# Kernel tuning notes

Hardware: AMD Instinct MI355X
Metric: run time of the kernel (lower is better)

## Reference

```python
import jax, jax.numpy as jnp
import numpy as np

IMG = 416
NC = 80
B = 32
NOBJ = 20          # objects placed per image
K = 32             # fixed max GT boxes per image for ignore-mask IoU (>= NOBJ)
THR = 0.5
ANCHORS = np.array([[10,13],[16,30],[33,23],[30,61],[62,45],[59,119],
                    [116,90],[156,198],[373,326]], np.float32)


def _bce(logits, targets):
    # elementwise binary_cross_entropy_with_logits
    return jnp.maximum(logits, 0.0) - logits * targets + jnp.log1p(jnp.exp(-jnp.abs(logits)))


def _make_y_true(key, batch, G, nc, img, nobj):
    N = G * G * 3
    k1, k2, k3, k4 = jax.random.split(key, 4)
    idx = jax.random.randint(k1, (batch, nobj), 0, N)
    xy = jax.random.uniform(k2, (batch, nobj, 2), jnp.float32) * img
    wh = jax.random.uniform(k3, (batch, nobj, 2), jnp.float32) * 90.0 + 10.0
    cls = jax.random.randint(k4, (batch, nobj), 0, nc)
    y = jnp.zeros((batch, N, 5 + nc), jnp.float32)
    b = jnp.arange(batch)[:, None]
    y = y.at[b, idx, 0].set(xy[..., 0])
    y = y.at[b, idx, 1].set(xy[..., 1])
    y = y.at[b, idx, 2].set(wh[..., 0])
    y = y.at[b, idx, 3].set(wh[..., 1])
    y = y.at[b, idx, 4].set(1.0)
    y = y.at[b, idx, 5 + cls].set(1.0)
    return y.reshape(batch, G, G, 3, 5 + nc)


def setup_inputs() -> dict:
    key = jax.random.key(0)
    ks = jax.random.split(key, 6)
    inp = {}
    for i, G in enumerate([13, 26, 52]):
        inp[f"fm{i}"] = jax.random.normal(ks[i], (B, 3 * (5 + NC), G, G), jnp.float32)
        inp[f"yt{i}"] = _make_y_true(ks[3 + i], B, G, NC, IMG, NOBJ)
    inp["anchors"] = jnp.asarray(ANCHORS)
    return inp


def _predict_transform(fm, anchors3):
    batch, ch, G, _ = fm.shape
    A = 3
    stride = IMG // G
    bbox = 5 + NC
    # [B, A*bbox, G*G] -> [B, G*G, A*bbox] -> [B, G, G, A, bbox]
    p = fm.reshape(batch, A * bbox, G * G).transpose(0, 2, 1).reshape(batch, G, G, A, bbox)
    box_centers = jax.nn.sigmoid(p[..., 0:2])
    box_sizes_raw = p[..., 2:4]
    conf_logits = p[..., 4:5]
    prob_logits = p[..., 5:]
    ar = jnp.arange(G, dtype=fm.dtype)
    gy, gx = jnp.meshgrid(ar, ar, indexing='ij')       # row, col
    xy_offset = jnp.stack([gx, gy], axis=-1).reshape(G, G, 1, 2)
    box_centers = (box_centers + xy_offset) * stride
    box_sizes = jnp.exp(box_sizes_raw) * (anchors3 / stride) * stride
    boxes = jnp.concatenate([box_centers, box_sizes], axis=-1)
    return xy_offset, boxes, conf_logits, prob_logits


def _ignore_mask(boxes, yt):
    batch, G, _, A, _ = boxes.shape
    N = G * G * A
    pb = boxes.reshape(batch, N, 4)
    tb_all = yt[..., :4].reshape(batch, N, 4)
    obj = yt[..., 4].reshape(batch, N)
    vals, idx = jax.lax.top_k(obj, K)                  # pick up to K GT boxes
    valid = vals > 0                                    # [B,K]
    tb = jnp.take_along_axis(tb_all, idx[:, :, None], axis=1)  # [B,K,4]
    tb = jnp.where(valid[:, :, None], tb, 0.0)
    p_xy = pb[:, :, None, 0:2]; p_wh = pb[:, :, None, 2:4]     # [B,N,1,2]
    t_xy = tb[:, None, :, 0:2]; t_wh = tb[:, None, :, 2:4]     # [B,1,K,2]
    mins = jnp.maximum(p_xy - p_wh / 2.0, t_xy - t_wh / 2.0)
    maxs = jnp.minimum(p_xy + p_wh / 2.0, t_xy + t_wh / 2.0)
    iwh = jnp.maximum(maxs - mins, 0.0)
    inter = iwh[..., 0] * iwh[..., 1]                  # [B,N,K]
    p_area = p_wh[..., 0] * p_wh[..., 1]
    t_area = t_wh[..., 0] * t_wh[..., 1]
    iou = inter / (p_area + t_area - inter + 1e-10)
    iou = jnp.where(valid[:, None, :], iou, 0.0)
    best_iou = jnp.max(iou, axis=-1)                   # [B,N]
    ign = (best_iou < THR).astype(boxes.dtype)
    # original: images with no valid GT boxes keep ignore_mask = 0
    ign = jnp.where(jnp.any(valid, axis=-1)[:, None], ign, 0.0)
    return ign.reshape(batch, G, G, A, 1)


def _calculate_one(fm, yt, anchors3):
    G = fm.shape[2]
    batch = yt.shape[0]
    ratio = IMG / G
    xy_offset, boxes, conf_logits, prob_logits = _predict_transform(fm, anchors3)
    object_mask = yt[..., 4:5]
    ignore_mask = _ignore_mask(boxes, yt)
    true_xy = yt[..., 0:2] / ratio - xy_offset
    pred_xy = boxes[..., 0:2] / ratio - xy_offset
    true_tw = yt[..., 2:4] / anchors3
    pred_tw = boxes[..., 2:4] / anchors3
    true_tw = jnp.where(true_tw == 0.0, 1.0, true_tw)
    pred_tw = jnp.where(pred_tw == 0.0, 1.0, pred_tw)
    true_tw = jnp.log(jnp.clip(true_tw, 1e-9, 1e9))
    pred_tw = jnp.log(jnp.clip(pred_tw, 1e-9, 1e9))
    box_scale = 2.0 - (yt[..., 2:3] / IMG) * (yt[..., 3:4] / IMG)
    xy_loss = 5.0 * jnp.sum((true_xy - pred_xy) ** 2 * object_mask * box_scale) / batch
    wh_loss = 5.0 * jnp.sum((true_tw - pred_tw) ** 2 * object_mask * box_scale) / batch
    bce_conf = _bce(conf_logits, object_mask)
    conf_loss = object_mask * bce_conf + 0.5 * (1.0 - object_mask) * ignore_mask * bce_conf
    focal = jnp.abs(object_mask - jax.nn.sigmoid(conf_logits)) ** 2.0   # alpha=1, gamma=2
    conf_loss = jnp.sum(conf_loss * focal) / batch
    delta = 0.01
    label_target = (1.0 - delta) * yt[..., 5:] + delta / NC
    class_loss = jnp.sum(object_mask * _bce(prob_logits, label_target)) / batch
    return xy_loss, wh_loss, conf_loss, class_loss


def reference(fm0, fm1, fm2, yt0, yt1, yt2, anchors):
    anchor_groups = [anchors[6:9], anchors[3:6], anchors[0:3]]
    fms = [fm0, fm1, fm2]
    yts = [yt0, yt1, yt2]
    xy = wh = conf = prob = 0.0
    for fm, yt, a3 in zip(fms, yts, anchor_groups):
        l_xy, l_wh, l_conf, l_prob = _calculate_one(fm, yt, a3)
        xy = xy + l_xy; wh = wh + l_wh; conf = conf + l_conf; prob = prob + l_prob
    total = xy + wh + conf + prob
    return (total, xy, wh, conf, prob)
```

## Files before the change

kernel.cpp:

```cpp
#include <hip/hip_runtime.h>
#include <math.h>


constexpr int   NCLS  = 80;
constexpr int   PMAX  = 4;
constexpr int   SLOTS = 32;
constexpr float IMGF  = 416.0f;

constexpr int NBLK_COLLECT = 32 * (1 + 2 + 4);
constexpr int NBLK_POS  = 768;
constexpr int NBLK_CONF = 96 + 288 + 1056;
constexpr int NBLK_MAIN = NBLK_POS + NBLK_CONF;

constexpr size_t OFF_CNT  = 0;
constexpr size_t OFF_PART = 1536;
constexpr size_t OFF_TGT  = OFF_PART + (size_t)NBLK_MAIN * 16;
constexpr size_t OFF_TGTN = OFF_TGT + (size_t)96 * PMAX * SLOTS * 16;

__device__ inline float sigmoidf_(float x) { return 1.0f / (1.0f + expf(-x)); }
__device__ inline float bcef_(float l, float t) {
    return fmaxf(l, 0.0f) - l * t + log1pf(expf(-fabsf(l)));
}

__global__ __launch_bounds__(512) void k_collect(
        const float* __restrict__ yt0, const float* __restrict__ yt1,
        const float* __restrict__ yt2,
        int* __restrict__ cnt, float* __restrict__ tgt, int* __restrict__ tgtn) {
    int bid = blockIdx.x, tid = threadIdx.x;
    int lane = tid & 63, wid = tid >> 6;
    int s, b, p, P, G;
    const float* yt;
    if (bid < 32)      { s = 0; b = bid;            p = 0;       P = 1; yt = yt0; G = 13; }
    else if (bid < 96) { s = 1; int i = bid - 32; b = i >> 1; p = i & 1; P = 2; yt = yt1; G = 26; }
    else               { s = 2; int i = bid - 96; b = i >> 2; p = i & 3; P = 4; yt = yt2; G = 52; }
    int GG3  = 3 * G * G;
    int per  = (GG3 + P - 1) / P;
    int nbase = p * per;
    int count = min(per, GG3 - nbase);
    int nit  = (count + 511) / 512;
    int sb = s * 32 + b;

    __shared__ int s_wcnt[8];
    __shared__ int s_base;
    if (tid == 0) s_base = 0;

    float obj[4];
    int   nn[4];
    #pragma unroll
    for (int it = 0; it < 4; ++it) {
        int c = it * 512 + tid;
        nn[it]  = nbase + c;
        obj[it] = 0.0f;
        if (c < count) obj[it] = yt[(size_t)(b * GG3 + nn[it]) * 85 + 4];
    }
    __syncthreads();

    for (int it = 0; it < nit; ++it) {
        bool pos = obj[it] > 0.5f;
        unsigned long long mask = __ballot(pos);
        if (lane == 0) s_wcnt[wid] = __popcll(mask);
        __syncthreads();
        int wpre = 0, tot = 0;
        #pragma unroll
        for (int w = 0; w < 8; ++w) { if (w < wid) wpre += s_wcnt[w]; tot += s_wcnt[w]; }
        int rank = s_base + wpre + (int)__popcll(mask & ((1ull << lane) - 1ull));
        if (pos && rank < SLOTS) {
            size_t yb = (size_t)(b * GG3 + nn[it]) * 85;
            int slot = (sb * PMAX + p) * SLOTS + rank;
            float4 box = make_float4(yt[yb], yt[yb + 1], yt[yb + 2], yt[yb + 3]);
            reinterpret_cast<float4*>(tgt)[slot] = box;
            tgtn[slot] = nn[it];
        }
        __syncthreads();
        if (tid == 0) s_base += tot;
        __syncthreads();
    }
    if (tid == 0) {
        cnt[sb * PMAX + p] = min(s_base, SLOTS);
        if (p == 0)
            for (int q = P; q < PMAX; ++q) cnt[sb * PMAX + q] = 0;
    }
}

__global__ __launch_bounds__(256) void k_main(
        const float* __restrict__ fm0, const float* __restrict__ fm1,
        const float* __restrict__ fm2,
        const float* __restrict__ yt0, const float* __restrict__ yt1,
        const float* __restrict__ yt2,
        const float* __restrict__ anch,
        const int* __restrict__ cnt, const float* __restrict__ tgt,
        const int* __restrict__ tgtn, float4* __restrict__ part) {
    __shared__ float  s_minx[128], s_maxx[128], s_miny[128], s_maxy[128], s_area[128];
    __shared__ int    s_tn[128];
    __shared__ int    s_cn4[4];
    __shared__ float4 s_w[4];

    int bid = blockIdx.x;
    int tid = threadIdx.x;
    int wid = tid >> 6, lane = tid & 63;

    float ax = 0.f, aw2 = 0.f, ap = 0.f, ac = 0.f;

    if (bid < NBLK_POS) {
        int slot = bid * 4 + wid;
        int sb = slot >> 5, idx = slot & 31;
        int s = sb >> 5, b = sb & 31;
        const float *fm, *yt;
        int G, anchoff;
        if (s == 0)      { fm = fm0; yt = yt0; G = 13; anchoff = 6; }
        else if (s == 1) { fm = fm1; yt = yt1; G = 26; anchoff = 3; }
        else             { fm = fm2; yt = yt2; G = 52; anchoff = 0; }
        int c0 = cnt[sb * PMAX + 0], c1 = cnt[sb * PMAX + 1];
        int c2 = cnt[sb * PMAX + 2], c3 = cnt[sb * PMAX + 3];
        int cn_total = c0 + c1 + c2 + c3;
        if (idx < cn_total) {
            int p = 0, rem = idx;
            if (rem >= c0) { rem -= c0; p = 1;
                if (rem >= c1) { rem -= c1; p = 2;
                    if (rem >= c2) { rem -= c2; p = 3; } } }
            int entry = (sb * PMAX + p) * SLOTS + rem;
            int GG = G * G;
            float stridef = IMGF / (float)G;
            float4 tb = reinterpret_cast<const float4*>(tgt)[entry];
            int n  = tgtn[entry];
            int a  = n % 3;
            int sp = n / 3;
            int jj = sp % G, ii = sp / G;
            int ybase = (b * 3 * GG + n) * 85;
            int fbase = (b * 255 + a * 85) * GG + sp;
            for (int c = lane; c < NCLS; c += 64) {
                float pl  = fm[fbase + (5 + c) * GG];
                float tl  = yt[ybase + 5 + c];
                float lab = 0.99f * tl + 1.25e-4f;
                ap += bcef_(pl, lab);
            }
            if (lane == 0) {
                float p0 = fm[fbase];
                float p1 = fm[fbase + GG];
                float p2 = fm[fbase + 2 * GG];
                float p3 = fm[fbase + 3 * GG];
                float bcx = (sigmoidf_(p0) + (float)jj) * stridef;
                float bcy = (sigmoidf_(p1) + (float)ii) * stridef;
                float predx = bcx / stridef - (float)jj;
                float predy = bcy / stridef - (float)ii;
                float truex = tb.x / stridef - (float)jj;
                float truey = tb.y / stridef - (float)ii;
                float dx = truex - predx, dy = truey - predy;
                float bscale = 2.0f - (tb.z / IMGF) * (tb.w / IMGF);
                float aw = anch[(anchoff + a) * 2], ah = anch[(anchoff + a) * 2 + 1];
                float pw = expf(p2) * (aw / stridef) * stridef;
                float ph = expf(p3) * (ah / stridef) * stridef;
                float ptw = pw / aw, pth = ph / ah;
                float ttw = tb.z / aw, tth = tb.w / ah;
                ttw = (ttw == 0.0f) ? 1.0f : ttw;
                tth = (tth == 0.0f) ? 1.0f : tth;
                ptw = (ptw == 0.0f) ? 1.0f : ptw;
                pth = (pth == 0.0f) ? 1.0f : pth;
                ttw = logf(fminf(fmaxf(ttw, 1e-9f), 1e9f));
                tth = logf(fminf(fmaxf(tth, 1e-9f), 1e9f));
                ptw = logf(fminf(fmaxf(ptw, 1e-9f), 1e9f));
                pth = logf(fminf(fmaxf(pth, 1e-9f), 1e9f));
                float dw = ttw - ptw, dh = tth - pth;
                ax  += (dx * dx + dy * dy) * bscale;
                aw2 += (dw * dw + dh * dh) * bscale;
            }
        }
    } else {
        int cb = bid - NBLK_POS;
        const float *fm;
        int G, chunks, s, anchoff;
        if (cb < 96)       { fm = fm0; G = 13; chunks = 1;  s = 0; anchoff = 6; }
        else if (cb < 384) { cb -= 96;  fm = fm1; G = 26; chunks = 3;  s = 1; anchoff = 3; }
        else               { cb -= 384; fm = fm2; G = 52; chunks = 11; s = 2; anchoff = 0; }
        int chunk = cb % chunks;
        int ba    = cb / chunks;
        int b = ba / 3, a = ba % 3;
        int GG = G * G;
        float stridef = IMGF / (float)G;
        int sb = s * 32 + b;
        if (tid < 4) s_cn4[tid] = cnt[sb * PMAX + tid];
        if (tid < 128) {
            int slot = sb * PMAX * SLOTS + tid;
            float4 tb = reinterpret_cast<const float4*>(tgt)[slot];
            s_minx[tid] = tb.x - tb.z * 0.5f;
            s_maxx[tid] = tb.x + tb.z * 0.5f;
            s_miny[tid] = tb.y - tb.w * 0.5f;
            s_maxy[tid] = tb.y + tb.w * 0.5f;
            s_area[tid] = tb.z * tb.w;
            s_tn[tid]   = tgtn[slot];
        }
        __syncthreads();
        int sp = chunk * 256 + tid;
        if (sp < GG) {
            int jj = sp % G, ii = sp / G;
            int n = sp * 3 + a;
            int fbase = (b * 255 + a * 85) * GG + sp;
            float p0 = fm[fbase];
            float p1 = fm[fbase + GG];
            float p2 = fm[fbase + 2 * GG];
            float p3 = fm[fbase + 3 * GG];
            float p4 = fm[fbase + 4 * GG];
            float aw = anch[(anchoff + a) * 2], ah = anch[(anchoff + a) * 2 + 1];
            float cx = (sigmoidf_(p0) + (float)jj) * stridef;
            float cy = (sigmoidf_(p1) + (float)ii) * stridef;
            float pw = expf(p2) * (aw / stridef) * stridef;
            float ph = expf(p3) * (ah / stridef) * stridef;
            float pminx = cx - pw * 0.5f, pmaxx = cx + pw * 0.5f;
            float pminy = cy - ph * 0.5f, pmaxy = cy + ph * 0.5f;
            float parea = pw * ph;
            float best = 0.0f, m = 0.0f;
            int cn_total = 0;
            #pragma unroll
            for (int p = 0; p < PMAX; ++p) {
                int cnp = s_cn4[p];
                cn_total += cnp;
                for (int k = 0; k < cnp; ++k) {
                    int e = p * SLOTS + k;
                    if (s_tn[e] == n) m = 1.0f;
                    float iw = fminf(pmaxx, s_maxx[e]) - fmaxf(pminx, s_minx[e]);
                    float ih = fminf(pmaxy, s_maxy[e]) - fmaxf(pminy, s_miny[e]);
                    iw = fmaxf(iw, 0.0f);
                    ih = fmaxf(ih, 0.0f);
                    float inter = iw * ih;
                    float iou = inter / ((parea + s_area[e] - inter) + 1e-10f);
                    best = fmaxf(best, iou);
                }
            }
            float ign = (cn_total > 0 && best < 0.5f) ? 1.0f : 0.0f;
            float bce = bcef_(p4, m);
            float d = fabsf(m - sigmoidf_(p4));
            ac += (m * bce + 0.5f * (1.0f - m) * ign * bce) * (d * d);
        }
    }

    for (int off = 32; off; off >>= 1) {
        ax  += __shfl_down(ax,  off);
        aw2 += __shfl_down(aw2, off);
        ap  += __shfl_down(ap,  off);
        ac  += __shfl_down(ac,  off);
    }
    if (lane == 0) s_w[wid] = make_float4(ax, aw2, ap, ac);
    __syncthreads();
    if (tid == 0) {
        float4 r0 = s_w[0], r1 = s_w[1], r2 = s_w[2], r3 = s_w[3];
        part[bid] = make_float4(r0.x + r1.x + r2.x + r3.x,
                                r0.y + r1.y + r2.y + r3.y,
                                r0.z + r1.z + r2.z + r3.z,
                                r0.w + r1.w + r2.w + r3.w);
    }
}

__global__ __launch_bounds__(512) void k_reduce(
        const float4* __restrict__ part, float* __restrict__ out) {
    int t = threadIdx.x;
    double x = 0.0, w = 0.0, p = 0.0, c = 0.0;
    for (int i = t; i < NBLK_MAIN; i += 512) {
        float4 v = part[i];
        x += (double)v.x; w += (double)v.y; p += (double)v.z; c += (double)v.w;
    }
    for (int off = 32; off; off >>= 1) {
        x += __shfl_down(x, off);
        w += __shfl_down(w, off);
        p += __shfl_down(p, off);
        c += __shfl_down(c, off);
    }
    __shared__ double sx[8], sw[8], sp[8], sc[8];
    int wid = t >> 6, lane = t & 63;
    if (lane == 0) { sx[wid] = x; sw[wid] = w; sp[wid] = p; sc[wid] = c; }
    __syncthreads();
    if (t == 0) {
        double X = 0, W = 0, P = 0, C = 0;
        for (int i = 0; i < 8; ++i) { X += sx[i]; W += sw[i]; P += sp[i]; C += sc[i]; }
        double xy = 5.0 * X / 32.0;
        double wh = 5.0 * W / 32.0;
        double cf = C / 32.0;
        double pb = P / 32.0;
        out[0] = (float)(xy + wh + cf + pb);
        out[1] = (float)xy;
        out[2] = (float)wh;
        out[3] = (float)cf;
        out[4] = (float)pb;
    }
}

extern "C" void kernel_launch(void* const* d_in, const int* in_sizes, int n_in,
                              void* d_out, int out_size, void* d_ws, size_t ws_size,
                              hipStream_t stream) {
    const float* fm0  = (const float*)d_in[0];
    const float* yt0  = (const float*)d_in[1];
    const float* fm1  = (const float*)d_in[2];
    const float* yt1  = (const float*)d_in[3];
    const float* fm2  = (const float*)d_in[4];
    const float* yt2  = (const float*)d_in[5];
    const float* anch = (const float*)d_in[6];
    float* out = (float*)d_out;

    char* ws = (char*)d_ws;
    int*    cnt  = (int*)(ws + OFF_CNT);
    float4* part = (float4*)(ws + OFF_PART);
    float*  tgt  = (float*)(ws + OFF_TGT);
    int*    tgtn = (int*)(ws + OFF_TGTN);

    k_collect<<<NBLK_COLLECT, 512, 0, stream>>>(yt0, yt1, yt2, cnt, tgt, tgtn);
    k_main<<<NBLK_MAIN, 256, 0, stream>>>(
        fm0, fm1, fm2, yt0, yt1, yt2, anch, cnt, tgt, tgtn, part);
    k_reduce<<<1, 512, 0, stream>>>(part, out);
}
```

Measured before the change: 35.40 us.

## Fuse positive-cell loss computation into collect kernel, split conf into own kernel

```diff
diff --git a/kernel.cpp b/kernel.cpp
--- a/kernel.cpp
+++ b/kernel.cpp
@@ -8,13 +8,12 @@
 constexpr float IMGF  = 416.0f;
 
 constexpr int NBLK_COLLECT = 32 * (1 + 2 + 4);
-constexpr int NBLK_POS  = 768;
-constexpr int NBLK_CONF = 96 + 288 + 1056;
-constexpr int NBLK_MAIN = NBLK_POS + NBLK_CONF;
+constexpr int NBLK_CONF    = 96 + 288 + 1056;
+constexpr int NPART        = NBLK_COLLECT + NBLK_CONF;
 
 constexpr size_t OFF_CNT  = 0;
 constexpr size_t OFF_PART = 1536;
-constexpr size_t OFF_TGT  = OFF_PART + (size_t)NBLK_MAIN * 16;
+constexpr size_t OFF_TGT  = OFF_PART + (size_t)NPART * 16;
 constexpr size_t OFF_TGTN = OFF_TGT + (size_t)96 * PMAX * SLOTS * 16;
 
 __device__ inline float sigmoidf_(float x) { return 1.0f / (1.0f + expf(-x)); }
@@ -23,25 +22,35 @@
 }
 
 __global__ __launch_bounds__(512) void k_collect(
+        const float* __restrict__ fm0, const float* __restrict__ fm1,
+        const float* __restrict__ fm2,
         const float* __restrict__ yt0, const float* __restrict__ yt1,
         const float* __restrict__ yt2,
-        int* __restrict__ cnt, float* __restrict__ tgt, int* __restrict__ tgtn) {
+        const float* __restrict__ anch,
+        int* __restrict__ cnt, float* __restrict__ tgt, int* __restrict__ tgtn,
+        float4* __restrict__ part) {
     int bid = blockIdx.x, tid = threadIdx.x;
     int lane = tid & 63, wid = tid >> 6;
     int s, b, p, P, G;
-    const float* yt;
-    if (bid < 32)      { s = 0; b = bid;            p = 0;       P = 1; yt = yt0; G = 13; }
-    else if (bid < 96) { s = 1; int i = bid - 32; b = i >> 1; p = i & 1; P = 2; yt = yt1; G = 26; }
-    else               { s = 2; int i = bid - 96; b = i >> 2; p = i & 3; P = 4; yt = yt2; G = 52; }
-    int GG3  = 3 * G * G;
+    const float *yt, *fm;
+    int anchoff;
+    if (bid < 32)      { s = 0; b = bid;          p = 0;       P = 1; yt = yt0; fm = fm0; G = 13; anchoff = 6; }
+    else if (bid < 96) { s = 1; int i = bid - 32; b = i >> 1; p = i & 1; P = 2; yt = yt1; fm = fm1; G = 26; anchoff = 3; }
+    else               { s = 2; int i = bid - 96; b = i >> 2; p = i & 3; P = 4; yt = yt2; fm = fm2; G = 52; anchoff = 0; }
+    int GG   = G * G;
+    int GG3  = 3 * GG;
     int per  = (GG3 + P - 1) / P;
     int nbase = p * per;
     int count = min(per, GG3 - nbase);
     int nit  = (count + 511) / 512;
     int sb = s * 32 + b;
-
-    __shared__ int s_wcnt[8];
-    __shared__ int s_base;
+    float stridef = IMGF / (float)G;
+
+    __shared__ int    s_wcnt[8];
+    __shared__ int    s_base;
+    __shared__ int    s_n[SLOTS];
+    __shared__ float4 s_box[SLOTS];
+    __shared__ float4 s_pw[8];
     if (tid == 0) s_base = 0;
 
     float obj[4];
@@ -70,191 +79,173 @@
             float4 box = make_float4(yt[yb], yt[yb + 1], yt[yb + 2], yt[yb + 3]);
             reinterpret_cast<float4*>(tgt)[slot] = box;
             tgtn[slot] = nn[it];
+            s_box[rank] = box;
+            s_n[rank]   = nn[it];
         }
         __syncthreads();
         if (tid == 0) s_base += tot;
         __syncthreads();
     }
+    int cn = min(s_base, SLOTS);
     if (tid == 0) {
-        cnt[sb * PMAX + p] = min(s_base, SLOTS);
+        cnt[sb * PMAX + p] = cn;
         if (p == 0)
             for (int q = P; q < PMAX; ++q) cnt[sb * PMAX + q] = 0;
     }
-}
-
-__global__ __launch_bounds__(256) void k_main(
+
+    float ax = 0.f, aw2 = 0.f, ap = 0.f;
+    for (int slot = wid; slot < cn; slot += 8) {
+        float4 tb = s_box[slot];
+        int n  = s_n[slot];
+        int a  = n % 3;
+        int sp = n / 3;
+        int jj = sp % G, ii = sp / G;
+        int ybase = (b * GG3 + n) * 85;
+        int fbase = (b * 255 + a * 85) * GG + sp;
+        for (int c = lane; c < NCLS; c += 64) {
+            float pl  = fm[fbase + (5 + c) * GG];
+            float tl  = yt[ybase + 5 + c];
+            float lab = 0.99f * tl + 1.25e-4f;
+            ap += bcef_(pl, lab);
+        }
+        if (lane == 0) {
+            float p0 = fm[fbase];
+            float p1 = fm[fbase + GG];
+            float p2 = fm[fbase + 2 * GG];
+            float p3 = fm[fbase + 3 * GG];
+            float bcx = (sigmoidf_(p0) + (float)jj) * stridef;
+            float bcy = (sigmoidf_(p1) + (float)ii) * stridef;
+            float predx = bcx / stridef - (float)jj;
+            float predy = bcy / stridef - (float)ii;
+            float truex = tb.x / stridef - (float)jj;
+            float truey = tb.y / stridef - (float)ii;
+            float dx = truex - predx, dy = truey - predy;
+            float bscale = 2.0f - (tb.z / IMGF) * (tb.w / IMGF);
+            float aw = anch[(anchoff + a) * 2], ah = anch[(anchoff + a) * 2 + 1];
+            float pw = expf(p2) * (aw / stridef) * stridef;
+            float ph = expf(p3) * (ah / stridef) * stridef;
+            float ptw = pw / aw, pth = ph / ah;
+            float ttw = tb.z / aw, tth = tb.w / ah;
+            ttw = (ttw == 0.0f) ? 1.0f : ttw;
+            tth = (tth == 0.0f) ? 1.0f : tth;
+            ptw = (ptw == 0.0f) ? 1.0f : ptw;
+            pth = (pth == 0.0f) ? 1.0f : pth;
+            ttw = logf(fminf(fmaxf(ttw, 1e-9f), 1e9f));
+            tth = logf(fminf(fmaxf(tth, 1e-9f), 1e9f));
+            ptw = logf(fminf(fmaxf(ptw, 1e-9f), 1e9f));
+            pth = logf(fminf(fmaxf(pth, 1e-9f), 1e9f));
+            float dw = ttw - ptw, dh = tth - pth;
+            ax  += (dx * dx + dy * dy) * bscale;
+            aw2 += (dw * dw + dh * dh) * bscale;
+        }
+    }
+    for (int off = 32; off; off >>= 1) ap += __shfl_down(ap, off);
+    if (lane == 0) s_pw[wid] = make_float4(ax, aw2, ap, 0.f);
+    __syncthreads();
+    if (tid == 0) {
+        float X = 0.f, W = 0.f, Pp = 0.f;
+        #pragma unroll
+        for (int w = 0; w < 8; ++w) { X += s_pw[w].x; W += s_pw[w].y; Pp += s_pw[w].z; }
+        part[bid] = make_float4(X, W, Pp, 0.f);
+    }
+}
+
+__global__ __launch_bounds__(256) void k_conf(
         const float* __restrict__ fm0, const float* __restrict__ fm1,
         const float* __restrict__ fm2,
-        const float* __restrict__ yt0, const float* __restrict__ yt1,
-        const float* __restrict__ yt2,
         const float* __restrict__ anch,
         const int* __restrict__ cnt, const float* __restrict__ tgt,
         const int* __restrict__ tgtn, float4* __restrict__ part) {
     __shared__ float  s_minx[128], s_maxx[128], s_miny[128], s_maxy[128], s_area[128];
     __shared__ int    s_tn[128];
     __shared__ int    s_cn4[4];
-    __shared__ float4 s_w[4];
+    __shared__ float  s_w1[4];
 
     int bid = blockIdx.x;
     int tid = threadIdx.x;
     int wid = tid >> 6, lane = tid & 63;
 
-    float ax = 0.f, aw2 = 0.f, ap = 0.f, ac = 0.f;
-
-    if (bid < NBLK_POS) {
-        int slot = bid * 4 + wid;
-        int sb = slot >> 5, idx = slot & 31;
-        int s = sb >> 5, b = sb & 31;
-        const float *fm, *yt;
-        int G, anchoff;
-        if (s == 0)      { fm = fm0; yt = yt0; G = 13; anchoff = 6; }
-        else if (s == 1) { fm = fm1; yt = yt1; G = 26; anchoff = 3; }
-        else             { fm = fm2; yt = yt2; G = 52; anchoff = 0; }
-        int c0 = cnt[sb * PMAX + 0], c1 = cnt[sb * PMAX + 1];
-        int c2 = cnt[sb * PMAX + 2], c3 = cnt[sb * PMAX + 3];
-        int cn_total = c0 + c1 + c2 + c3;
-        if (idx < cn_total) {
-            int p = 0, rem = idx;
-            if (rem >= c0) { rem -= c0; p = 1;
-                if (rem >= c1) { rem -= c1; p = 2;
-                    if (rem >= c2) { rem -= c2; p = 3; } } }
-            int entry = (sb * PMAX + p) * SLOTS + rem;
-            int GG = G * G;
-            float stridef = IMGF / (float)G;
-            float4 tb = reinterpret_cast<const float4*>(tgt)[entry];
-            int n  = tgtn[entry];
-            int a  = n % 3;
-            int sp = n / 3;
-            int jj = sp % G, ii = sp / G;
-            int ybase = (b * 3 * GG + n) * 85;
-            int fbase = (b * 255 + a * 85) * GG + sp;
-            for (int c = lane; c < NCLS; c += 64) {
-                float pl  = fm[fbase + (5 + c) * GG];
-                float tl  = yt[ybase + 5 + c];
-                float lab = 0.99f * tl + 1.25e-4f;
-                ap += bcef_(pl, lab);
-            }
-            if (lane == 0) {
-                float p0 = fm[fbase];
-                float p1 = fm[fbase + GG];
-                float p2 = fm[fbase + 2 * GG];
-                float p3 = fm[fbase + 3 * GG];
-                float bcx = (sigmoidf_(p0) + (float)jj) * stridef;
-                float bcy = (sigmoidf_(p1) + (float)ii) * stridef;
-                float predx = bcx / stridef - (float)jj;
-                float predy = bcy / stridef - (float)ii;
-                float truex = tb.x / stridef - (float)jj;
-                float truey = tb.y / stridef - (float)ii;
-                float dx = truex - predx, dy = truey - predy;
-                float bscale = 2.0f - (tb.z / IMGF) * (tb.w / IMGF);
-                float aw = anch[(anchoff + a) * 2], ah = anch[(anchoff + a) * 2 + 1];
-                float pw = expf(p2) * (aw / stridef) * stridef;
-                float ph = expf(p3) * (ah / stridef) * stridef;
-                float ptw = pw / aw, pth = ph / ah;
-                float ttw = tb.z / aw, tth = tb.w / ah;
-                ttw = (ttw == 0.0f) ? 1.0f : ttw;
-                tth = (tth == 0.0f) ? 1.0f : tth;
-                ptw = (ptw == 0.0f) ? 1.0f : ptw;
-                pth = (pth == 0.0f) ? 1.0f : pth;
-                ttw = logf(fminf(fmaxf(ttw, 1e-9f), 1e9f));
-                tth = logf(fminf(fmaxf(tth, 1e-9f), 1e9f));
-                ptw = logf(fminf(fmaxf(ptw, 1e-9f), 1e9f));
-                pth = logf(fminf(fmaxf(pth, 1e-9f), 1e9f));
-                float dw = ttw - ptw, dh = tth - pth;
-                ax  += (dx * dx + dy * dy) * bscale;
-                aw2 += (dw * dw + dh * dh) * bscale;
+    int cb = bid;
+    const float *fm;
+    int G, chunks, s, anchoff;
+    if (cb < 96)       { fm = fm0; G = 13; chunks = 1;  s = 0; anchoff = 6; }
+    else if (cb < 384) { cb -= 96;  fm = fm1; G = 26; chunks = 3;  s = 1; anchoff = 3; }
+    else               { cb -= 384; fm = fm2; G = 52; chunks = 11; s = 2; anchoff = 0; }
+    int chunk = cb % chunks;
+    int ba    = cb / chunks;
+    int b = ba / 3, a = ba % 3;
+    int GG = G * G;
+    float stridef = IMGF / (float)G;
+    int sb = s * 32 + b;
+    if (tid < 4) s_cn4[tid] = cnt[sb * PMAX + tid];
+    if (tid < 128) {
+        int slot = sb * PMAX * SLOTS + tid;
+        float4 tb = reinterpret_cast<const float4*>(tgt)[slot];
+        s_minx[tid] = tb.x - tb.z * 0.5f;
+        s_maxx[tid] = tb.x + tb.z * 0.5f;
+        s_miny[tid] = tb.y - tb.w * 0.5f;
+        s_maxy[tid] = tb.y + tb.w * 0.5f;
+        s_area[tid] = tb.z * tb.w;
+        s_tn[tid]   = tgtn[slot];
+    }
+    __syncthreads();
+
+    float ac = 0.f;
+    int sp = chunk * 256 + tid;
+    if (sp < GG) {
+        int jj = sp % G, ii = sp / G;
+        int n = sp * 3 + a;
+        int fbase = (b * 255 + a * 85) * GG + sp;
+        float p0 = fm[fbase];
+        float p1 = fm[fbase + GG];
+        float p2 = fm[fbase + 2 * GG];
+        float p3 = fm[fbase + 3 * GG];
+        float p4 = fm[fbase + 4 * GG];
+        float aw = anch[(anchoff + a) * 2], ah = anch[(anchoff + a) * 2 + 1];
+        float cx = (sigmoidf_(p0) + (float)jj) * stridef;
+        float cy = (sigmoidf_(p1) + (float)ii) * stridef;
+        float pw = expf(p2) * (aw / stridef) * stridef;
+        float ph = expf(p3) * (ah / stridef) * stridef;
+        float pminx = cx - pw * 0.5f, pmaxx = cx + pw * 0.5f;
+        float pminy = cy - ph * 0.5f, pmaxy = cy + ph * 0.5f;
+        float parea = pw * ph;
+        float best = 0.0f, m = 0.0f;
+        int cn_total = 0;
+        #pragma unroll
+        for (int pp = 0; pp < PMAX; ++pp) {
+            int cnp = s_cn4[pp];
+            cn_total += cnp;
+            for (int k = 0; k < cnp; ++k) {
+                int e = pp * SLOTS + k;
+                if (s_tn[e] == n) m = 1.0f;
+                float iw = fminf(pmaxx, s_maxx[e]) - fmaxf(pminx, s_minx[e]);
+                float ih = fminf(pmaxy, s_maxy[e]) - fmaxf(pminy, s_miny[e]);
+                iw = fmaxf(iw, 0.0f);
+                ih = fmaxf(ih, 0.0f);
+                float inter = iw * ih;
+                float iou = inter / ((parea + s_area[e] - inter) + 1e-10f);
+                best = fmaxf(best, iou);
             }
         }
-    } else {
-        int cb = bid - NBLK_POS;
-        const float *fm;
-        int G, chunks, s, anchoff;
-        if (cb < 96)       { fm = fm0; G = 13; chunks = 1;  s = 0; anchoff = 6; }
-        else if (cb < 384) { cb -= 96;  fm = fm1; G = 26; chunks = 3;  s = 1; anchoff = 3; }
-        else               { cb -= 384; fm = fm2; G = 52; chunks = 11; s = 2; anchoff = 0; }
-        int chunk = cb % chunks;
-        int ba    = cb / chunks;
-        int b = ba / 3, a = ba % 3;
-        int GG = G * G;
-        float stridef = IMGF / (float)G;
-        int sb = s * 32 + b;
-        if (tid < 4) s_cn4[tid] = cnt[sb * PMAX + tid];
-        if (tid < 128) {
-            int slot = sb * PMAX * SLOTS + tid;
-            float4 tb = reinterpret_cast<const float4*>(tgt)[slot];
-            s_minx[tid] = tb.x - tb.z * 0.5f;
-            s_maxx[tid] = tb.x + tb.z * 0.5f;
-            s_miny[tid] = tb.y - tb.w * 0.5f;
-            s_maxy[tid] = tb.y + tb.w * 0.5f;
-            s_area[tid] = tb.z * tb.w;
-            s_tn[tid]   = tgtn[slot];
-        }
-        __syncthreads();
-        int sp = chunk * 256 + tid;
-        if (sp < GG) {
-            int jj = sp % G, ii = sp / G;
-            int n = sp * 3 + a;
-            int fbase = (b * 255 + a * 85) * GG + sp;
-            float p0 = fm[fbase];
-            float p1 = fm[fbase + GG];
-            float p2 = fm[fbase + 2 * GG];
-            float p3 = fm[fbase + 3 * GG];
-            float p4 = fm[fbase + 4 * GG];
-            float aw = anch[(anchoff + a) * 2], ah = anch[(anchoff + a) * 2 + 1];
-            float cx = (sigmoidf_(p0) + (float)jj) * stridef;
-            float cy = (sigmoidf_(p1) + (float)ii) * stridef;
-            float pw = expf(p2) * (aw / stridef) * stridef;
-            float ph = expf(p3) * (ah / stridef) * stridef;
-            float pminx = cx - pw * 0.5f, pmaxx = cx + pw * 0.5f;
-            float pminy = cy - ph * 0.5f, pmaxy = cy + ph * 0.5f;
-            float parea = pw * ph;
-            float best = 0.0f, m = 0.0f;
-            int cn_total = 0;
-            #pragma unroll
-            for (int p = 0; p < PMAX; ++p) {
-                int cnp = s_cn4[p];
-                cn_total += cnp;
-                for (int k = 0; k < cnp; ++k) {
-                    int e = p * SLOTS + k;
-                    if (s_tn[e] == n) m = 1.0f;
-                    float iw = fminf(pmaxx, s_maxx[e]) - fmaxf(pminx, s_minx[e]);
-                    float ih = fminf(pmaxy, s_maxy[e]) - fmaxf(pminy, s_miny[e]);
-                    iw = fmaxf(iw, 0.0f);
-                    ih = fmaxf(ih, 0.0f);
-                    float inter = iw * ih;
-                    float iou = inter / ((parea + s_area[e] - inter) + 1e-10f);
-                    best = fmaxf(best, iou);
-                }
-            }
-            float ign = (cn_total > 0 && best < 0.5f) ? 1.0f : 0.0f;
-            float bce = bcef_(p4, m);
-            float d = fabsf(m - sigmoidf_(p4));
-            ac += (m * bce + 0.5f * (1.0f - m) * ign * bce) * (d * d);
-        }
-    }
-
-    for (int off = 32; off; off >>= 1) {
-        ax  += __shfl_down(ax,  off);
-        aw2 += __shfl_down(aw2, off);
-        ap  += __shfl_down(ap,  off);
-        ac  += __shfl_down(ac,  off);
-    }
-    if (lane == 0) s_w[wid] = make_float4(ax, aw2, ap, ac);
-    __syncthreads();
-    if (tid == 0) {
-        float4 r0 = s_w[0], r1 = s_w[1], r2 = s_w[2], r3 = s_w[3];
-        part[bid] = make_float4(r0.x + r1.x + r2.x + r3.x,
-                                r0.y + r1.y + r2.y + r3.y,
-                                r0.z + r1.z + r2.z + r3.z,
-                                r0.w + r1.w + r2.w + r3.w);
-    }
+        float ign = (cn_total > 0 && best < 0.5f) ? 1.0f : 0.0f;
+        float bce = bcef_(p4, m);
+        float d = fabsf(m - sigmoidf_(p4));
+        ac = (m * bce + 0.5f * (1.0f - m) * ign * bce) * (d * d);
+    }
+
+    for (int off = 32; off; off >>= 1) ac += __shfl_down(ac, off);
+    if (lane == 0) s_w1[wid] = ac;
+    __syncthreads();
+    if (tid == 0)
+        part[NBLK_COLLECT + bid] =
+            make_float4(0.f, 0.f, 0.f, s_w1[0] + s_w1[1] + s_w1[2] + s_w1[3]);
 }
 
 __global__ __launch_bounds__(512) void k_reduce(
         const float4* __restrict__ part, float* __restrict__ out) {
     int t = threadIdx.x;
     double x = 0.0, w = 0.0, p = 0.0, c = 0.0;
-    for (int i = t; i < NBLK_MAIN; i += 512) {
+    for (int i = t; i < NPART; i += 512) {
         float4 v = part[i];
         x += (double)v.x; w += (double)v.y; p += (double)v.z; c += (double)v.w;
     }
@@ -301,8 +292,9 @@
     float*  tgt  = (float*)(ws + OFF_TGT);
     int*    tgtn = (int*)(ws + OFF_TGTN);
 
-    k_collect<<<NBLK_COLLECT, 512, 0, stream>>>(yt0, yt1, yt2, cnt, tgt, tgtn);
-    k_main<<<NBLK_MAIN, 256, 0, stream>>>(
+    k_collect<<<NBLK_COLLECT, 512, 0, stream>>>(
         fm0, fm1, fm2, yt0, yt1, yt2, anch, cnt, tgt, tgtn, part);
+    k_conf<<<NBLK_CONF, 256, 0, stream>>>(
+        fm0, fm1, fm2, anch, cnt, tgt, tgtn, part);
     k_reduce<<<1, 512, 0, stream>>>(part, out);
 }
```

Measured after the change: 34.42 us (median of 2 runs). -2.8%, faster.
